# Optimization experiments

Measured on AMD Instinct MI355X. Metric: run time of the kernel, lower is better.

## Reference

```python
import jax, jax.numpy as jnp
import numpy as np

B, N, F, C, L = 8, 1024, 256, 256, 4


def setup_inputs() -> dict:
    key = jax.random.key(0)
    k1, k2, k3 = jax.random.split(key, 3)
    V = jax.random.normal(k1, (B, N, F), dtype=jnp.float32)
    A = jax.random.uniform(k2, (B, N, N, L), dtype=jnp.float32)
    # learned relational weights: (L+1, C, F); index 0 corresponds to the identity (self) edge
    h_weights = jax.random.normal(k3, (L + 1, C, F), dtype=jnp.float32) * 0.05
    return {"V": V, "A": A, "h_weights": h_weights}


def reference(V, A, h_weights):
    # out[b,i,c] = relu( sum_{l,j,f} A_aug[b,i,j,l] * h[l,c,f] * V[b,j,f] )
    # where A_aug = concat(I, A) on the last axis. We avoid materializing the
    # (B, N*C, N*F) intermediate of the naive impl by projecting V first.
    VW = jnp.einsum('bjf,lcf->bljc', V, h_weights)          # (B, L+1, N, C)
    # identity edge (l=0) contributes VW[:,0] directly; remaining L edge types aggregate over A
    out = VW[:, 0] + jnp.einsum('bijl,bljc->bic', A, VW[:, 1:])  # (B, N, C)
    return jax.nn.relu(out)
```

## Files before the change

### kernel.cpp

```cpp
#include <hip/hip_runtime.h>


typedef float          f32x4  __attribute__((ext_vector_type(4)));
typedef __bf16         bf16x8 __attribute__((ext_vector_type(8)));
typedef unsigned short u16x4  __attribute__((ext_vector_type(4)));
typedef unsigned int   u32x4  __attribute__((ext_vector_type(4)));

#define DEV __device__ __forceinline__

DEV void glds16(const void* g, void* l) {
  __builtin_amdgcn_global_load_lds((const __attribute__((address_space(1))) void*)g,
                                   (__attribute__((address_space(3))) void*)l,
                                   16, 0, 0);
}

DEV void cvt8(__bf16* d, f32x4 u, f32x4 v) {
  bf16x8 o;
  o[0]=(__bf16)u[0]; o[1]=(__bf16)u[1]; o[2]=(__bf16)u[2]; o[3]=(__bf16)u[3];
  o[4]=(__bf16)v[0]; o[5]=(__bf16)v[1]; o[6]=(__bf16)v[2]; o[7]=(__bf16)v[3];
  *(bf16x8*)d = o;
}

DEV unsigned short bfbits(float x) {
  return __builtin_bit_cast(unsigned short, (__bf16)x);
}

__global__ __launch_bounds__(512, 2)
void k1_vw(const float* __restrict__ Vg, const float* __restrict__ Hg,
           unsigned short* __restrict__ W2t, float* __restrict__ VW0)
{
  __shared__ __attribute__((aligned(16))) __bf16 Vs[2][128*64];
  __shared__ __attribute__((aligned(16))) __bf16 Hs[2][320*64];

  const int tid  = threadIdx.x;
  const int lane = tid & 63;
  const int wid  = tid >> 6;
  const int wj   = wid >> 1;
  const int wc   = wid & 1;
  const int li   = lane & 15;
  const int lg   = lane >> 4;

  const int bid = blockIdx.x;
  const int ct  = bid & 3;
  const int jt  = (bid >> 2) & 7;
  const int b   = bid >> 5;
  const int j0  = jt * 128;
  const int c0  = ct * 64;

  const float* sptr[7];
  int sdst[7];
#pragma unroll
  for (int r = 0; r < 2; ++r) {
    int n = r*512 + tid, row = n >> 3, q = n & 7;
    sptr[r] = Vg + (size_t)(b*1024 + j0 + row)*256 + q*8;
    sdst[r] = row*64 + ((q ^ (row & 7))*8);
  }
#pragma unroll
  for (int r = 0; r < 5; ++r) {
    int n = r*512 + tid, row = n >> 3, q = n & 7;
    int l = row >> 6, cl = row & 63;
    sptr[2+r] = Hg + (size_t)(l*256 + c0 + cl)*256 + q*8;
    sdst[2+r] = row*64 + ((q ^ (row & 7))*8);
  }

  f32x4 acc[5][2][2];
#pragma unroll
  for (int l=0;l<5;l++)
#pragma unroll
    for (int x=0;x<2;x++)
#pragma unroll
      for (int y=0;y<2;y++) acc[l][x][y] = (f32x4){0.f,0.f,0.f,0.f};

  {
    f32x4 sa[14];
#pragma unroll
    for (int i=0;i<7;i++) { sa[2*i] = *(const f32x4*)(sptr[i]); sa[2*i+1] = *(const f32x4*)(sptr[i]+4); }
#pragma unroll
    for (int i=0;i<7;i++) {
      __bf16* d = (i < 2) ? &Vs[0][sdst[i]] : &Hs[0][sdst[i]];
      cvt8(d, sa[2*i], sa[2*i+1]);
    }
  }
  __syncthreads();

  int cur = 0;
#pragma unroll 1
  for (int t = 0; t < 4; ++t) {
    const int nxt = cur ^ 1;
    f32x4 sa[14];
    if (t < 3) {
      const int ko = (t+1)*64;
#pragma unroll
      for (int i=0;i<7;i++) { sa[2*i] = *(const f32x4*)(sptr[i]+ko); sa[2*i+1] = *(const f32x4*)(sptr[i]+ko+4); }
    }
    const __bf16* Vsc = &Vs[cur][0];
    const __bf16* Hsc = &Hs[cur][0];
#pragma unroll
    for (int ks = 0; ks < 2; ++ks) {
      bf16x8 hf[10], vf[2];
#pragma unroll
      for (int l=0;l<5;l++)
#pragma unroll
        for (int cm=0;cm<2;cm++) {
          int row = l*64 + wc*32 + cm*16 + li;
          int ch  = (ks*4 + lg) ^ (row & 7);
          hf[l*2+cm] = *(const bf16x8*)(Hsc + row*64 + ch*8);
        }
#pragma unroll
      for (int jn=0;jn<2;jn++) {
        int row = wj*32 + jn*16 + li;
        int ch  = (ks*4 + lg) ^ (row & 7);
        vf[jn] = *(const bf16x8*)(Vsc + row*64 + ch*8);
      }
#pragma unroll
      for (int l=0;l<5;l++)
#pragma unroll
        for (int cm=0;cm<2;cm++)
#pragma unroll
          for (int jn=0;jn<2;jn++)
            acc[l][cm][jn] = __builtin_amdgcn_mfma_f32_16x16x32_bf16(
                hf[l*2+cm], vf[jn], acc[l][cm][jn], 0, 0, 0);
    }
    if (t < 3) {
#pragma unroll
      for (int i=0;i<7;i++) {
        __bf16* d = (i < 2) ? &Vs[nxt][sdst[i]] : &Hs[nxt][sdst[i]];
        cvt8(d, sa[2*i], sa[2*i+1]);
      }
    }
    __syncthreads();
    cur = nxt;
  }

#pragma unroll
  for (int cm=0;cm<2;cm++)
#pragma unroll
    for (int r=0;r<4;r++) {
      const int c = c0 + wc*32 + cm*16 + lg*4 + r;
#pragma unroll
      for (int jn=0;jn<2;jn++) {
        const int j = j0 + wj*32 + jn*16 + li;
        u16x4 pk;
        pk[0] = bfbits(acc[1][cm][jn][r]);
        pk[1] = bfbits(acc[2][cm][jn][r]);
        pk[2] = bfbits(acc[3][cm][jn][r]);
        pk[3] = bfbits(acc[4][cm][jn][r]);
        *(u16x4*)(W2t + (size_t)(b*256 + c)*4096 + (size_t)j*4) = pk;
        VW0[(size_t)(b*1024 + j)*256 + c] = acc[0][cm][jn][r];
      }
    }
}

template<int KT>
__global__ __launch_bounds__(512, 4)
void k2_gemm(const float* __restrict__ Ag, const unsigned short* __restrict__ W2t,
             unsigned short* __restrict__ part)
{
  __shared__ __attribute__((aligned(16))) __bf16 As[2][128*32];
  __shared__ __attribute__((aligned(16))) __bf16 Bs[2][256*32];

  constexpr int KCH   = 4096 / KT;
  constexpr int NSTEP = KCH / 32;

  const int tid  = threadIdx.x;
  const int lane = tid & 63;
  const int wid  = tid >> 6;
  const int wi   = wid >> 2;
  const int wc   = wid & 3;
  const int li   = lane & 15;
  const int lg   = lane >> 4;

  const int p   = blockIdx.x;
  const int bid = (p & 7) * (8*KT) + (p >> 3);
  const int kt  = bid % KT;
  const int it  = (bid / KT) & 7;
  const int b   = bid / (8*KT);

  const int i0 = it*128, k0 = kt*KCH;

  const int arow = tid >> 2, aq = tid & 3;
  const float* asrc = Ag + (size_t)(b*1024 + i0 + arow)*4096 + k0 + aq*8;
  const int ad = arow*32 + ((aq ^ ((arow >> 1) & 3))*8);

  const unsigned short *bsrc0, *bsrc1;
  {
    int n, row, q;
    n = tid;        row = n>>2; q = n&3;
    bsrc0 = W2t + (size_t)(b*256 + row)*4096 + k0 + ((q ^ ((row>>1)&3))*8);
    n = 512 + tid;  row = n>>2; q = n&3;
    bsrc1 = W2t + (size_t)(b*256 + row)*4096 + k0 + ((q ^ ((row>>1)&3))*8);
  }
  const int bd0 = wid*512;
  const int bd1 = 4096 + wid*512;

  f32x4 acc[4][4];
#pragma unroll
  for (int m=0;m<4;m++)
#pragma unroll
    for (int n=0;n<4;n++) acc[m][n] = (f32x4){0.f,0.f,0.f,0.f};

  {
    f32x4 a0 = *(const f32x4*)asrc, a1 = *(const f32x4*)(asrc+4);
    glds16(bsrc0, &Bs[0][bd0]);
    glds16(bsrc1, &Bs[0][bd1]);
    cvt8(&As[0][ad], a0, a1);
  }
  __syncthreads();

  int cur = 0;
#pragma unroll 1
  for (int t = 0; t < NSTEP; ++t) {
    const int nxt = cur ^ 1;
    f32x4 a0, a1;
    if (t < NSTEP-1) {
      const int o = (t+1)*32;
      a0 = *(const f32x4*)(asrc + o);
      a1 = *(const f32x4*)(asrc + o + 4);
      glds16(bsrc0 + o, &Bs[nxt][bd0]);
      glds16(bsrc1 + o, &Bs[nxt][bd1]);
    }
    {
      bf16x8 af[4], bfv[4];
#pragma unroll
      for (int m=0;m<4;m++) {
        int row = wi*64 + m*16 + li;
        int ch  = lg ^ ((row >> 1) & 3);
        af[m] = *(const bf16x8*)(&As[cur][row*32 + ch*8]);
      }
#pragma unroll
      for (int n=0;n<4;n++) {
        int row = wc*64 + n*16 + li;
        int ch  = lg ^ ((row >> 1) & 3);
        bfv[n] = *(const bf16x8*)(&Bs[cur][row*32 + ch*8]);
      }
#pragma unroll
      for (int m=0;m<4;m++)
#pragma unroll
        for (int n=0;n<4;n++)
          acc[m][n] = __builtin_amdgcn_mfma_f32_16x16x32_bf16(af[m], bfv[n], acc[m][n], 0, 0, 0);
    }
    if (t < NSTEP-1) cvt8(&As[nxt][ad], a0, a1);
    __syncthreads();
    cur = nxt;
  }

  unsigned short* pb = part + (size_t)kt*2097152u + (size_t)(b*1024 + i0)*256;
#pragma unroll
  for (int m=0;m<4;m++)
#pragma unroll
    for (int r=0;r<4;r++) {
      const int il = wi*64 + m*16 + lg*4 + r;
#pragma unroll
      for (int n=0;n<4;n++) {
        const int cl = wc*64 + n*16 + li;
        pb[(size_t)il*256 + cl] = bfbits(acc[m][n][r]);
      }
    }
}

template<int NP>
__global__ __launch_bounds__(256)
void k3_reduce(const unsigned short* __restrict__ part, const float* __restrict__ VW0,
               float* __restrict__ out)
{
  const size_t i8 = ((size_t)blockIdx.x*256 + threadIdx.x)*8;
  f32x4 s0 = *(const f32x4*)(VW0 + i8);
  f32x4 s1 = *(const f32x4*)(VW0 + i8 + 4);
#pragma unroll
  for (int p=0;p<NP;p++) {
    u32x4 u = *(const u32x4*)(part + (size_t)p*2097152u + i8);
    s0[0] += __uint_as_float(u[0] << 16);  s0[1] += __uint_as_float(u[0] & 0xffff0000u);
    s0[2] += __uint_as_float(u[1] << 16);  s0[3] += __uint_as_float(u[1] & 0xffff0000u);
    s1[0] += __uint_as_float(u[2] << 16);  s1[1] += __uint_as_float(u[2] & 0xffff0000u);
    s1[2] += __uint_as_float(u[3] << 16);  s1[3] += __uint_as_float(u[3] & 0xffff0000u);
  }
#pragma unroll
  for (int e=0;e<4;e++){ s0[e] = fmaxf(s0[e],0.f); s1[e] = fmaxf(s1[e],0.f); }
  *(f32x4*)(out + i8)     = s0;
  *(f32x4*)(out + i8 + 4) = s1;
}

extern "C" void kernel_launch(void* const* d_in, const int* in_sizes, int n_in,
                              void* d_out, int out_size, void* d_ws, size_t ws_size,
                              hipStream_t stream) {
  const float* Vg = (const float*)d_in[0];
  const float* Ag = (const float*)d_in[1];
  const float* Hg = (const float*)d_in[2];
  float* out = (float*)d_out;

  if (ws_size < 41943040u) return;
  char* ws = (char*)d_ws;
  unsigned short* W2t  = (unsigned short*)(ws);
  float*          VW0  = (float*)(ws + 16777216u);
  unsigned short* part = (unsigned short*)(ws + 16777216u + 8388608u);

  const bool big = (ws_size >= 58720256u);

  k1_vw<<<dim3(256), dim3(512), 0, stream>>>(Vg, Hg, W2t, VW0);
  if (big) {
    k2_gemm<8><<<dim3(512), dim3(512), 0, stream>>>(Ag, W2t, part);
    k3_reduce<8><<<dim3(1024), dim3(256), 0, stream>>>(part, VW0, out);
  } else {
    k2_gemm<4><<<dim3(256), dim3(512), 0, stream>>>(Ag, W2t, part);
    k3_reduce<4><<<dim3(1024), dim3(256), 0, stream>>>(part, VW0, out);
  }
}
```

Measured before the change: 56.60 us.

## Shrink GEMM tile to 64 rows, 256 threads, and map batches round-robin

```diff
diff --git a/kernel.cpp b/kernel.cpp
--- a/kernel.cpp
+++ b/kernel.cpp
@@ -40,12 +40,13 @@
   const int li   = lane & 15;
   const int lg   = lane >> 4;
 
-  const int bid = blockIdx.x;
-  const int ct  = bid & 3;
-  const int jt  = (bid >> 2) & 7;
-  const int b   = bid >> 5;
-  const int j0  = jt * 128;
-  const int c0  = ct * 64;
+  const int p    = blockIdx.x;
+  const int b    = p & 7;
+  const int rest = p >> 3;
+  const int ct   = rest & 3;
+  const int jt   = rest >> 2;
+  const int j0   = jt * 128;
+  const int c0   = ct * 64;
 
   const float* sptr[7];
   int sdst[7];
@@ -151,47 +152,43 @@
     }
 }
 
-template<int KT>
-__global__ __launch_bounds__(512, 4)
+__global__ __launch_bounds__(256, 4)
 void k2_gemm(const float* __restrict__ Ag, const unsigned short* __restrict__ W2t,
              unsigned short* __restrict__ part)
 {
-  __shared__ __attribute__((aligned(16))) __bf16 As[2][128*32];
+  __shared__ __attribute__((aligned(16))) __bf16 As[2][64*32];
   __shared__ __attribute__((aligned(16))) __bf16 Bs[2][256*32];
 
+  constexpr int KT    = 8;
   constexpr int KCH   = 4096 / KT;
   constexpr int NSTEP = KCH / 32;
 
   const int tid  = threadIdx.x;
   const int lane = tid & 63;
-  const int wid  = tid >> 6;
-  const int wi   = wid >> 2;
-  const int wc   = wid & 3;
+  const int wc   = tid >> 6;
   const int li   = lane & 15;
   const int lg   = lane >> 4;
 
-  const int p   = blockIdx.x;
-  const int bid = (p & 7) * (8*KT) + (p >> 3);
-  const int kt  = bid % KT;
-  const int it  = (bid / KT) & 7;
-  const int b   = bid / (8*KT);
-
-  const int i0 = it*128, k0 = kt*KCH;
+  const int p    = blockIdx.x;
+  const int b    = p & 7;
+  const int rest = p >> 3;
+  const int kt   = rest & 7;
+  const int it   = rest >> 3;
+
+  const int i0 = it*64, k0 = kt*KCH;
 
   const int arow = tid >> 2, aq = tid & 3;
   const float* asrc = Ag + (size_t)(b*1024 + i0 + arow)*4096 + k0 + aq*8;
   const int ad = arow*32 + ((aq ^ ((arow >> 1) & 3))*8);
 
-  const unsigned short *bsrc0, *bsrc1;
-  {
-    int n, row, q;
-    n = tid;        row = n>>2; q = n&3;
-    bsrc0 = W2t + (size_t)(b*256 + row)*4096 + k0 + ((q ^ ((row>>1)&3))*8);
-    n = 512 + tid;  row = n>>2; q = n&3;
-    bsrc1 = W2t + (size_t)(b*256 + row)*4096 + k0 + ((q ^ ((row>>1)&3))*8);
-  }
-  const int bd0 = wid*512;
-  const int bd1 = 4096 + wid*512;
+  const unsigned short* bsrc[4];
+  int bd[4];
+#pragma unroll
+  for (int r = 0; r < 4; ++r) {
+    int n = r*256 + tid, row = n >> 2, q = n & 3;
+    bsrc[r] = W2t + (size_t)(b*256 + row)*4096 + k0 + ((q ^ ((row>>1)&3))*8);
+    bd[r]   = r*2048 + wc*512;
+  }
 
   f32x4 acc[4][4];
 #pragma unroll
@@ -201,8 +198,8 @@
 
   {
     f32x4 a0 = *(const f32x4*)asrc, a1 = *(const f32x4*)(asrc+4);
-    glds16(bsrc0, &Bs[0][bd0]);
-    glds16(bsrc1, &Bs[0][bd1]);
+#pragma unroll
+    for (int r=0;r<4;r++) glds16(bsrc[r], &Bs[0][bd[r]]);
     cvt8(&As[0][ad], a0, a1);
   }
   __syncthreads();
@@ -216,14 +213,14 @@
       const int o = (t+1)*32;
       a0 = *(const f32x4*)(asrc + o);
       a1 = *(const f32x4*)(asrc + o + 4);
-      glds16(bsrc0 + o, &Bs[nxt][bd0]);
-      glds16(bsrc1 + o, &Bs[nxt][bd1]);
+#pragma unroll
+      for (int r=0;r<4;r++) glds16(bsrc[r] + o, &Bs[nxt][bd[r]]);
     }
     {
       bf16x8 af[4], bfv[4];
 #pragma unroll
       for (int m=0;m<4;m++) {
-        int row = wi*64 + m*16 + li;
+        int row = m*16 + li;
         int ch  = lg ^ ((row >> 1) & 3);
         af[m] = *(const bf16x8*)(&As[cur][row*32 + ch*8]);
       }
@@ -249,7 +246,7 @@
   for (int m=0;m<4;m++)
 #pragma unroll
     for (int r=0;r<4;r++) {
-      const int il = wi*64 + m*16 + lg*4 + r;
+      const int il = m*16 + lg*4 + r;
 #pragma unroll
       for (int n=0;n<4;n++) {
         const int cl = wc*64 + n*16 + li;
@@ -258,17 +255,19 @@
     }
 }
 
-template<int NP>
 __global__ __launch_bounds__(256)
 void k3_reduce(const unsigned short* __restrict__ part, const float* __restrict__ VW0,
                float* __restrict__ out)
 {
-  const size_t i8 = ((size_t)blockIdx.x*256 + threadIdx.x)*8;
+  const int p   = blockIdx.x;
+  const int b   = p & 7;
+  const int off = p >> 3;
+  const size_t i8 = (size_t)b*262144u + (size_t)off*2048u + (size_t)threadIdx.x*8;
   f32x4 s0 = *(const f32x4*)(VW0 + i8);
   f32x4 s1 = *(const f32x4*)(VW0 + i8 + 4);
 #pragma unroll
-  for (int p=0;p<NP;p++) {
-    u32x4 u = *(const u32x4*)(part + (size_t)p*2097152u + i8);
+  for (int q=0;q<8;q++) {
+    u32x4 u = *(const u32x4*)(part + (size_t)q*2097152u + i8);
     s0[0] += __uint_as_float(u[0] << 16);  s0[1] += __uint_as_float(u[0] & 0xffff0000u);
     s0[2] += __uint_as_float(u[1] << 16);  s0[3] += __uint_as_float(u[1] & 0xffff0000u);
     s1[0] += __uint_as_float(u[2] << 16);  s1[1] += __uint_as_float(u[2] & 0xffff0000u);
@@ -288,20 +287,13 @@
   const float* Hg = (const float*)d_in[2];
   float* out = (float*)d_out;
 
-  if (ws_size < 41943040u) return;
+  if (ws_size < 58720256u) return;
   char* ws = (char*)d_ws;
   unsigned short* W2t  = (unsigned short*)(ws);
   float*          VW0  = (float*)(ws + 16777216u);
   unsigned short* part = (unsigned short*)(ws + 16777216u + 8388608u);
 
-  const bool big = (ws_size >= 58720256u);
-
-  k1_vw<<<dim3(256), dim3(512), 0, stream>>>(Vg, Hg, W2t, VW0);
-  if (big) {
-    k2_gemm<8><<<dim3(512), dim3(512), 0, stream>>>(Ag, W2t, part);
-    k3_reduce<8><<<dim3(1024), dim3(256), 0, stream>>>(part, VW0, out);
-  } else {
-    k2_gemm<4><<<dim3(256), dim3(512), 0, stream>>>(Ag, W2t, part);
-    k3_reduce<4><<<dim3(1024), dim3(256), 0, stream>>>(part, VW0, out);
-  }
-}
+  k1_vw    <<<dim3(256),  dim3(512), 0, stream>>>(Vg, Hg, W2t, VW0);
+  k2_gemm  <<<dim3(1024), dim3(256), 0, stream>>>(Ag, W2t, part);
+  k3_reduce<<<dim3(1024), dim3(256), 0, stream>>>(part, VW0, out);
+}
```

New measurement: 62.55 us. 10.5% more time.
